# Kernel tuning notes

Measured on AMD Instinct MI355X. Metric: run time of the kernel, lower is better.

The kernel has to match this reference:

```python
import jax, jax.numpy as jnp
import numpy as np

N, F_IN, F_OUT = 8192, 512, 256


def setup_inputs() -> dict:
    key = jax.random.key(0)
    k1, k2, k3, k4 = jax.random.split(key, 4)
    x = jax.random.normal(k1, (N, F_IN), dtype=jnp.float32)
    adj = jax.random.randint(k2, (N, N), 0, 2, dtype=jnp.int32)
    # xavier_uniform with gain=1.414
    limW = 1.414 * np.sqrt(6.0 / (F_IN + F_OUT))
    W = jax.random.uniform(k3, (F_IN, F_OUT), dtype=jnp.float32, minval=-limW, maxval=limW)
    lima = 1.414 * np.sqrt(6.0 / (2 * F_OUT + 1))
    a = jax.random.uniform(k4, (2 * F_OUT, 1), dtype=jnp.float32, minval=-lima, maxval=lima)
    return {"x": x, "adj": adj, "W": W, "a": a}


def reference(x, adj, W, a):
    # h = x @ W : [N, F_out]
    h = x @ W
    f_out = h.shape[1]
    # additive score a^T [h_i ; h_j] is separable: (h @ a_l)_i + (h @ a_r)_j
    f_src = h @ a[:f_out, 0]   # [N]
    f_dst = h @ a[f_out:, 0]   # [N]
    e = jax.nn.leaky_relu(f_src[:, None] + f_dst[None, :], negative_slope=0.2)  # [N, N]
    e = jnp.where(adj > 0, e, jnp.float32(-9e15))
    attention = jax.nn.softmax(e, axis=1)  # row-wise over neighbors
    # dropout(p=0.6) is identity in eval mode
    h_prime = attention @ h  # [N, F_out]
    return h_prime
```

## Files before the change

kernel.cpp:

```cpp
#include <hip/hip_runtime.h>
#include <hip/hip_bf16.h>

#define NN 8192
#define FIN 512
#define FOUT 256

typedef __attribute__((ext_vector_type(8))) short short8;
typedef __attribute__((ext_vector_type(4))) short short4v;
typedef __attribute__((ext_vector_type(4))) float float4v;

__device__ __forceinline__ short f2bf(float f) {
    union { float f; unsigned u; } v; v.f = f;
    unsigned r = (v.u + 0x7FFFu + ((v.u >> 16) & 1u)) >> 16;
    return (short)r;
}
__device__ __forceinline__ float bf2f(short b) {
    union { unsigned u; float f; } v; v.u = ((unsigned)(unsigned short)b) << 16;
    return v.f;
}

__global__ __launch_bounds__(256) void wt_kernel(const float* __restrict__ W,
                                                 short* __restrict__ Wt) {
    int idx = blockIdx.x * 256 + threadIdx.x;
    int n = idx >> 9, k = idx & 511;
    Wt[idx] = f2bf(W[k * FOUT + n]);
}

__global__ __launch_bounds__(256) void h_kernel(const float* __restrict__ x,
                                                const short* __restrict__ Wt,
                                                short* __restrict__ h_t) {
    int wave = (blockIdx.x << 2) + (threadIdx.x >> 6);
    int lane = threadIdx.x & 63;
    int m0 = (wave & 511) << 4;
    int n0 = (wave >> 9) << 6;
    int lr = lane & 15, lq = lane >> 4;

    const float* xrow = x + (size_t)(m0 + lr) * FIN + lq * 8;
    const short* wbase = Wt + (size_t)(n0 + lr) * FIN + lq * 8;

    float4v acc[4] = {};
    for (int k0 = 0; k0 < FIN; k0 += 32) {
        float4v xa = *(const float4v*)(xrow + k0);
        float4v xb = *(const float4v*)(xrow + k0 + 4);
        short8 a;
        a[0] = f2bf(xa[0]); a[1] = f2bf(xa[1]); a[2] = f2bf(xa[2]); a[3] = f2bf(xa[3]);
        a[4] = f2bf(xb[0]); a[5] = f2bf(xb[1]); a[6] = f2bf(xb[2]); a[7] = f2bf(xb[3]);
#pragma unroll
        for (int ct = 0; ct < 4; ct++) {
            short8 b = *(const short8*)(wbase + (size_t)ct * 16 * FIN + k0);
            acc[ct] = __builtin_amdgcn_mfma_f32_16x16x32_bf16(a, b, acc[ct], 0, 0, 0);
        }
    }
#pragma unroll
    for (int ct = 0; ct < 4; ct++) {
#pragma unroll
        for (int reg = 0; reg < 4; reg++) {
            int m = m0 + lq * 4 + reg;
            int n = n0 + ct * 16 + lr;
            h_t[(size_t)n * NN + m] = f2bf(acc[ct][reg]);
        }
    }
}

__global__ __launch_bounds__(256) void f_kernel(const short* __restrict__ h_t,
                                                const float* __restrict__ a,
                                                float* __restrict__ f_src,
                                                float* __restrict__ f_dst) {
    int i = blockIdx.x * 256 + threadIdx.x;
    float s = 0.f, d = 0.f;
#pragma unroll 4
    for (int n = 0; n < FOUT; n++) {
        float hv = bf2f(h_t[(size_t)n * NN + i]);
        s = fmaf(hv, a[n], s);
        d = fmaf(hv, a[FOUT + n], d);
    }
    const float LOG2E = 1.4426950408889634f;
    f_src[i] = s * LOG2E;
    f_dst[i] = d * LOG2E;
}

__global__ __launch_bounds__(512) void gat_kernel(const int* __restrict__ adj,
                                                  const short* __restrict__ h_t,
                                                  const float* __restrict__ f_src,
                                                  const float* __restrict__ f_dst,
                                                  float* __restrict__ out) {
    __shared__ short Pt[32 * 72];
    __shared__ short Ht[256 * 72];
    __shared__ float l_sm[32];

    const int t = threadIdx.x;
    const int i0 = blockIdx.x * 32;
    const int r = t >> 4;
    const int c = t & 15;
    const int lane = t & 63;
    const int w = t >> 6;
    const int lr = lane & 15, lq = lane >> 4;
    const int n0 = w * 32;

    const float fs = f_src[i0 + r];
    const int* adjRow = adj + (size_t)(i0 + r) * NN + c * 4;

    float lpart = 0.f;
    float4v acc[2][2] = {};

    int4 av = *(const int4*)(adjRow);
    float4 fd = *(const float4*)(f_dst + c * 4);

    for (int j0 = 0; j0 < NN; j0 += 64) {
        float p[4];
        const float* fdp = (const float*)&fd;
        const int* avp = (const int*)&av;
#pragma unroll
        for (int q = 0; q < 4; q++) {
            float y = fs + fdp[q];
            y = fmaxf(y, 0.2f * y);
            float e = exp2f(y);
            p[q] = (avp[q] != 0) ? e : 0.f;
            lpart += p[q];
        }
        short4v pb;
        pb[0] = f2bf(p[0]); pb[1] = f2bf(p[1]); pb[2] = f2bf(p[2]); pb[3] = f2bf(p[3]);
        *(short4v*)&Pt[r * 72 + c * 4] = pb;

#pragma unroll
        for (int q = 0; q < 4; q++) {
            int c2 = t + q * 512;
            int n = c2 >> 3, ko = (c2 & 7) * 8;
            *(int4*)&Ht[n * 72 + ko] = *(const int4*)(h_t + (size_t)n * NN + j0 + ko);
        }

        if (j0 + 64 < NN) {
            av = *(const int4*)(adjRow + j0 + 64);
            fd = *(const float4*)(f_dst + j0 + 64 + c * 4);
        }
        __syncthreads();

#pragma unroll
        for (int kk = 0; kk < 2; kk++) {
            short8 a0 = *(const short8*)&Pt[lr * 72 + kk * 32 + lq * 8];
            short8 a1 = *(const short8*)&Pt[(16 + lr) * 72 + kk * 32 + lq * 8];
            short8 b0 = *(const short8*)&Ht[(n0 + lr) * 72 + kk * 32 + lq * 8];
            short8 b1 = *(const short8*)&Ht[(n0 + 16 + lr) * 72 + kk * 32 + lq * 8];
            acc[0][0] = __builtin_amdgcn_mfma_f32_16x16x32_bf16(a0, b0, acc[0][0], 0, 0, 0);
            acc[0][1] = __builtin_amdgcn_mfma_f32_16x16x32_bf16(a0, b1, acc[0][1], 0, 0, 0);
            acc[1][0] = __builtin_amdgcn_mfma_f32_16x16x32_bf16(a1, b0, acc[1][0], 0, 0, 0);
            acc[1][1] = __builtin_amdgcn_mfma_f32_16x16x32_bf16(a1, b1, acc[1][1], 0, 0, 0);
        }
        __syncthreads();
    }

#pragma unroll
    for (int off = 8; off >= 1; off >>= 1) lpart += __shfl_xor(lpart, off);
    if (c == 0) l_sm[r] = lpart;
    __syncthreads();

#pragma unroll
    for (int rt = 0; rt < 2; rt++) {
#pragma unroll
        for (int ct = 0; ct < 2; ct++) {
#pragma unroll
            for (int reg = 0; reg < 4; reg++) {
                int m = rt * 16 + lq * 4 + reg;
                int n = n0 + ct * 16 + lr;
                out[(size_t)(i0 + m) * FOUT + n] = acc[rt][ct][reg] / l_sm[m];
            }
        }
    }
}

extern "C" void kernel_launch(void* const* d_in, const int* in_sizes, int n_in,
                              void* d_out, int out_size, void* d_ws, size_t ws_size,
                              hipStream_t stream) {
    const float* x   = (const float*)d_in[0];
    const int*   adj = (const int*)d_in[1];
    const float* W   = (const float*)d_in[2];
    const float* a   = (const float*)d_in[3];
    float* out = (float*)d_out;

    char* ws = (char*)d_ws;
    short* h_t   = (short*)ws;
    short* Wt    = (short*)(ws + (4u << 20));
    float* f_src = (float*)(ws + (4u << 20) + (256u << 10));
    float* f_dst = (float*)(ws + (4u << 20) + (288u << 10));

    wt_kernel<<<512, 256, 0, stream>>>(W, Wt);
    h_kernel<<<512, 256, 0, stream>>>(x, Wt, h_t);
    f_kernel<<<NN / 256, 256, 0, stream>>>(h_t, a, f_src, f_dst);
    gat_kernel<<<NN / 32, 512, 0, stream>>>(adj, h_t, f_src, f_dst, out);
}
```

Measured before the change: 473.5 us.

## Split-K GAT aggregation with 64-row tiles, 32x32 MFMA, fused score projection

The main attention kernel now processes 64 query rows per block using 32x32x16 bf16 MFMAs. The neighbor dimension is split into up to four slices, with partial numerators and denominators written to workspace and summed by a new combine kernel. The f_src/f_dst projection is fused into the h GEMM epilogue using shuffles and atomics, removing a separate kernel. The W transpose now goes through shared memory so its accesses coalesce. The split adds partial-output traffic and an extra launch in exchange for more parallelism and higher reuse of h tiles across rows.

Measured after the change: 448.1 us. 1.06x faster.

```diff
diff --git a/kernel.cpp b/kernel.cpp
--- a/kernel.cpp
+++ b/kernel.cpp
@@ -4,31 +4,39 @@
 #define NN 8192
 #define FIN 512
 #define FOUT 256
+#define JTILE 64
 
 typedef __attribute__((ext_vector_type(8))) short short8;
 typedef __attribute__((ext_vector_type(4))) short short4v;
 typedef __attribute__((ext_vector_type(4))) float float4v;
+typedef __attribute__((ext_vector_type(16))) float float16v;
 
 __device__ __forceinline__ short f2bf(float f) {
     union { float f; unsigned u; } v; v.f = f;
     unsigned r = (v.u + 0x7FFFu + ((v.u >> 16) & 1u)) >> 16;
     return (short)r;
 }
-__device__ __forceinline__ float bf2f(short b) {
-    union { unsigned u; float f; } v; v.u = ((unsigned)(unsigned short)b) << 16;
-    return v.f;
-}
 
 __global__ __launch_bounds__(256) void wt_kernel(const float* __restrict__ W,
                                                  short* __restrict__ Wt) {
-    int idx = blockIdx.x * 256 + threadIdx.x;
-    int n = idx >> 9, k = idx & 511;
-    Wt[idx] = f2bf(W[k * FOUT + n]);
+    __shared__ short tile[32][33];
+    int tx = threadIdx.x & 31, ty = threadIdx.x >> 5;
+    int k0 = blockIdx.x * 32, n0 = blockIdx.y * 32;
+#pragma unroll
+    for (int r = 0; r < 32; r += 8)
+        tile[ty + r][tx] = f2bf(W[(size_t)(k0 + ty + r) * FOUT + n0 + tx]);
+    __syncthreads();
+#pragma unroll
+    for (int r = 0; r < 32; r += 8)
+        Wt[(size_t)(n0 + ty + r) * FIN + k0 + tx] = tile[tx][ty + r];
 }
 
 __global__ __launch_bounds__(256) void h_kernel(const float* __restrict__ x,
                                                 const short* __restrict__ Wt,
-                                                short* __restrict__ h_t) {
+                                                const float* __restrict__ a,
+                                                short* __restrict__ h_t,
+                                                float* __restrict__ f_src,
+                                                float* __restrict__ f_dst) {
     int wave = (blockIdx.x << 2) + (threadIdx.x >> 6);
     int lane = threadIdx.x & 63;
     int m0 = (wave & 511) << 4;
@@ -42,130 +50,164 @@
     for (int k0 = 0; k0 < FIN; k0 += 32) {
         float4v xa = *(const float4v*)(xrow + k0);
         float4v xb = *(const float4v*)(xrow + k0 + 4);
-        short8 a;
-        a[0] = f2bf(xa[0]); a[1] = f2bf(xa[1]); a[2] = f2bf(xa[2]); a[3] = f2bf(xa[3]);
-        a[4] = f2bf(xb[0]); a[5] = f2bf(xb[1]); a[6] = f2bf(xb[2]); a[7] = f2bf(xb[3]);
+        short8 av;
+        av[0] = f2bf(xa[0]); av[1] = f2bf(xa[1]); av[2] = f2bf(xa[2]); av[3] = f2bf(xa[3]);
+        av[4] = f2bf(xb[0]); av[5] = f2bf(xb[1]); av[6] = f2bf(xb[2]); av[7] = f2bf(xb[3]);
 #pragma unroll
         for (int ct = 0; ct < 4; ct++) {
-            short8 b = *(const short8*)(wbase + (size_t)ct * 16 * FIN + k0);
-            acc[ct] = __builtin_amdgcn_mfma_f32_16x16x32_bf16(a, b, acc[ct], 0, 0, 0);
-        }
-    }
+            short8 bv = *(const short8*)(wbase + (size_t)ct * 16 * FIN + k0);
+            acc[ct] = __builtin_amdgcn_mfma_f32_16x16x32_bf16(av, bv, acc[ct], 0, 0, 0);
+        }
+    }
+    float s_part[4] = {0.f, 0.f, 0.f, 0.f};
+    float d_part[4] = {0.f, 0.f, 0.f, 0.f};
 #pragma unroll
     for (int ct = 0; ct < 4; ct++) {
+        int n = n0 + ct * 16 + lr;
+        float al = a[n], ar = a[FOUT + n];
 #pragma unroll
         for (int reg = 0; reg < 4; reg++) {
-            int m = m0 + lq * 4 + reg;
-            int n = n0 + ct * 16 + lr;
-            h_t[(size_t)n * NN + m] = f2bf(acc[ct][reg]);
-        }
-    }
-}
-
-__global__ __launch_bounds__(256) void f_kernel(const short* __restrict__ h_t,
-                                                const float* __restrict__ a,
-                                                float* __restrict__ f_src,
-                                                float* __restrict__ f_dst) {
-    int i = blockIdx.x * 256 + threadIdx.x;
-    float s = 0.f, d = 0.f;
-#pragma unroll 4
-    for (int n = 0; n < FOUT; n++) {
-        float hv = bf2f(h_t[(size_t)n * NN + i]);
-        s = fmaf(hv, a[n], s);
-        d = fmaf(hv, a[FOUT + n], d);
+            float hv = acc[ct][reg];
+            s_part[reg] = fmaf(hv, al, s_part[reg]);
+            d_part[reg] = fmaf(hv, ar, d_part[reg]);
+            h_t[(size_t)n * NN + (m0 + lq * 4 + reg)] = f2bf(hv);
+        }
+    }
+#pragma unroll
+    for (int off = 1; off < 16; off <<= 1) {
+#pragma unroll
+        for (int reg = 0; reg < 4; reg++) {
+            s_part[reg] += __shfl_xor(s_part[reg], off);
+            d_part[reg] += __shfl_xor(d_part[reg], off);
+        }
     }
     const float LOG2E = 1.4426950408889634f;
-    f_src[i] = s * LOG2E;
-    f_dst[i] = d * LOG2E;
-}
-
-__global__ __launch_bounds__(512) void gat_kernel(const int* __restrict__ adj,
-                                                  const short* __restrict__ h_t,
-                                                  const float* __restrict__ f_src,
-                                                  const float* __restrict__ f_dst,
-                                                  float* __restrict__ out) {
-    __shared__ short Pt[32 * 72];
+    if (lr == 0) {
+#pragma unroll
+        for (int reg = 0; reg < 4; reg++) {
+            atomicAdd(&f_src[m0 + lq * 4 + reg], s_part[reg] * LOG2E);
+            atomicAdd(&f_dst[m0 + lq * 4 + reg], d_part[reg] * LOG2E);
+        }
+    }
+}
+
+__global__ __launch_bounds__(256, 2) void gat_kernel(const int* __restrict__ adj,
+                                                     const short* __restrict__ h_t,
+                                                     const float* __restrict__ f_src,
+                                                     const float* __restrict__ f_dst,
+                                                     float* __restrict__ Opart,
+                                                     float* __restrict__ lpart,
+                                                     int jlen) {
     __shared__ short Ht[256 * 72];
-    __shared__ float l_sm[32];
+    __shared__ short Pt[64 * 72];
+    __shared__ float Fd[2][64];
 
     const int t = threadIdx.x;
-    const int i0 = blockIdx.x * 32;
-    const int r = t >> 4;
-    const int c = t & 15;
-    const int lane = t & 63;
-    const int w = t >> 6;
-    const int lr = lane & 15, lq = lane >> 4;
-    const int n0 = w * 32;
-
-    const float fs = f_src[i0 + r];
-    const int* adjRow = adj + (size_t)(i0 + r) * NN + c * 4;
-
-    float lpart = 0.f;
-    float4v acc[2][2] = {};
-
-    int4 av = *(const int4*)(adjRow);
-    float4 fd = *(const float4*)(f_dst + c * 4);
-
-    for (int j0 = 0; j0 < NN; j0 += 64) {
-        float p[4];
-        const float* fdp = (const float*)&fd;
-        const int* avp = (const int*)&av;
-#pragma unroll
-        for (int q = 0; q < 4; q++) {
-            float y = fs + fdp[q];
-            y = fmaxf(y, 0.2f * y);
-            float e = exp2f(y);
-            p[q] = (avp[q] != 0) ? e : 0.f;
-            lpart += p[q];
-        }
-        short4v pb;
-        pb[0] = f2bf(p[0]); pb[1] = f2bf(p[1]); pb[2] = f2bf(p[2]); pb[3] = f2bf(p[3]);
-        *(short4v*)&Pt[r * 72 + c * 4] = pb;
-
-#pragma unroll
-        for (int q = 0; q < 4; q++) {
-            int c2 = t + q * 512;
-            int n = c2 >> 3, ko = (c2 & 7) * 8;
-            *(int4*)&Ht[n * 72 + ko] = *(const int4*)(h_t + (size_t)n * NN + j0 + ko);
-        }
-
-        if (j0 + 64 < NN) {
-            av = *(const int4*)(adjRow + j0 + 64);
-            fd = *(const float4*)(f_dst + j0 + 64 + c * 4);
+    const int i0 = blockIdx.x * 64;
+    const int slice = blockIdx.y;
+    const int jbase = slice * jlen;
+
+    const int prow = t >> 2, pjq = t & 3;
+    const int lane = t & 63, w = t >> 6;
+    const int l31 = lane & 31, lq = lane >> 5;
+    const int wn0 = w * 64;
+
+    const float fs = f_src[i0 + prow];
+    const int* adjRow = adj + (size_t)(i0 + prow) * NN;
+    const short* hrow = h_t + ((size_t)t << 13);
+
+    float16v acc00 = {}, acc01 = {}, acc10 = {}, acc11 = {};
+    float lp = 0.f;
+
+    if (t < 16) *(float4*)&Fd[0][t * 4] = *(const float4*)(f_dst + jbase + t * 4);
+    int4 av0 = *(const int4*)(adjRow + jbase + pjq * 16);
+    int4 av1 = *(const int4*)(adjRow + jbase + pjq * 16 + 4);
+    int4 av2 = *(const int4*)(adjRow + jbase + pjq * 16 + 8);
+    int4 av3 = *(const int4*)(adjRow + jbase + pjq * 16 + 12);
+    __syncthreads();
+
+    int buf = 0;
+    for (int jo = 0; jo < jlen; jo += JTILE) {
+        const int j0 = jbase + jo;
+        {
+            const float* fdc = &Fd[buf][pjq * 16];
+            short8 pbl, pbh;
+            int4 avs[4] = {av0, av1, av2, av3};
+#pragma unroll
+            for (int g = 0; g < 4; g++) {
+                const int* ai = (const int*)&avs[g];
+#pragma unroll
+                for (int q = 0; q < 4; q++) {
+                    float y = fs + fdc[g * 4 + q];
+                    y = fmaxf(y, 0.2f * y);
+                    float e = exp2f(y);
+                    float p = (ai[q] != 0) ? e : 0.f;
+                    lp += p;
+                    short pb = f2bf(p);
+                    if (g < 2) pbl[g * 4 + q] = pb; else pbh[(g - 2) * 4 + q] = pb;
+                }
+            }
+            *(short8*)&Pt[prow * 72 + pjq * 16] = pbl;
+            *(short8*)&Pt[prow * 72 + pjq * 16 + 8] = pbh;
+        }
+#pragma unroll
+        for (int q = 0; q < 8; q++)
+            *(short8*)&Ht[t * 72 + q * 8] = *(const short8*)(hrow + j0 + q * 8);
+
+        if (jo + JTILE < jlen) {
+            if (t < 16) *(float4*)&Fd[buf ^ 1][t * 4] = *(const float4*)(f_dst + j0 + JTILE + t * 4);
+            av0 = *(const int4*)(adjRow + j0 + JTILE + pjq * 16);
+            av1 = *(const int4*)(adjRow + j0 + JTILE + pjq * 16 + 4);
+            av2 = *(const int4*)(adjRow + j0 + JTILE + pjq * 16 + 8);
+            av3 = *(const int4*)(adjRow + j0 + JTILE + pjq * 16 + 12);
         }
         __syncthreads();
 
 #pragma unroll
-        for (int kk = 0; kk < 2; kk++) {
-            short8 a0 = *(const short8*)&Pt[lr * 72 + kk * 32 + lq * 8];
-            short8 a1 = *(const short8*)&Pt[(16 + lr) * 72 + kk * 32 + lq * 8];
-            short8 b0 = *(const short8*)&Ht[(n0 + lr) * 72 + kk * 32 + lq * 8];
-            short8 b1 = *(const short8*)&Ht[(n0 + 16 + lr) * 72 + kk * 32 + lq * 8];
-            acc[0][0] = __builtin_amdgcn_mfma_f32_16x16x32_bf16(a0, b0, acc[0][0], 0, 0, 0);
-            acc[0][1] = __builtin_amdgcn_mfma_f32_16x16x32_bf16(a0, b1, acc[0][1], 0, 0, 0);
-            acc[1][0] = __builtin_amdgcn_mfma_f32_16x16x32_bf16(a1, b0, acc[1][0], 0, 0, 0);
-            acc[1][1] = __builtin_amdgcn_mfma_f32_16x16x32_bf16(a1, b1, acc[1][1], 0, 0, 0);
-        }
+        for (int kk = 0; kk < 4; kk++) {
+            short8 a0 = *(const short8*)&Pt[l31 * 72 + kk * 16 + lq * 8];
+            short8 a1 = *(const short8*)&Pt[(32 + l31) * 72 + kk * 16 + lq * 8];
+            short8 b0 = *(const short8*)&Ht[(wn0 + l31) * 72 + kk * 16 + lq * 8];
+            short8 b1 = *(const short8*)&Ht[(wn0 + 32 + l31) * 72 + kk * 16 + lq * 8];
+            acc00 = __builtin_amdgcn_mfma_f32_32x32x16_bf16(a0, b0, acc00, 0, 0, 0);
+            acc01 = __builtin_amdgcn_mfma_f32_32x32x16_bf16(a0, b1, acc01, 0, 0, 0);
+            acc10 = __builtin_amdgcn_mfma_f32_32x32x16_bf16(a1, b0, acc10, 0, 0, 0);
+            acc11 = __builtin_amdgcn_mfma_f32_32x32x16_bf16(a1, b1, acc11, 0, 0, 0);
+        }
+        buf ^= 1;
         __syncthreads();
     }
 
-#pragma unroll
-    for (int off = 8; off >= 1; off >>= 1) lpart += __shfl_xor(lpart, off);
-    if (c == 0) l_sm[r] = lpart;
-    __syncthreads();
-
+    lp += __shfl_xor(lp, 1);
+    lp += __shfl_xor(lp, 2);
+    if (pjq == 0) lpart[slice * NN + i0 + prow] = lp;
+
+    float* obase = Opart + ((size_t)slice * NN + i0) * FOUT;
 #pragma unroll
     for (int rt = 0; rt < 2; rt++) {
 #pragma unroll
-        for (int ct = 0; ct < 2; ct++) {
-#pragma unroll
-            for (int reg = 0; reg < 4; reg++) {
-                int m = rt * 16 + lq * 4 + reg;
-                int n = n0 + ct * 16 + lr;
-                out[(size_t)(i0 + m) * FOUT + n] = acc[rt][ct][reg] / l_sm[m];
+        for (int nt = 0; nt < 2; nt++) {
+            const float16v& av = rt == 0 ? (nt == 0 ? acc00 : acc01) : (nt == 0 ? acc10 : acc11);
+#pragma unroll
+            for (int reg = 0; reg < 16; reg++) {
+                int row = rt * 32 + (reg & 3) + 8 * (reg >> 2) + 4 * lq;
+                int n = wn0 + nt * 32 + l31;
+                obase[(size_t)row * FOUT + n] = av[reg];
             }
         }
     }
+}
+
+__global__ __launch_bounds__(256) void combine_kernel(const float* __restrict__ Opart,
+                                                      const float* __restrict__ lpart,
+                                                      float* __restrict__ out, int slices) {
+    int i = blockIdx.x, n = threadIdx.x;
+    float o = 0.f, l = 0.f;
+    for (int s = 0; s < slices; s++) {
+        o += Opart[((size_t)s * NN + i) * FOUT + n];
+        l += lpart[s * NN + i];
+    }
+    out[(size_t)i * FOUT + n] = o / l;
 }
 
 extern "C" void kernel_launch(void* const* d_in, const int* in_sizes, int n_in,
@@ -182,9 +224,19 @@
     short* Wt    = (short*)(ws + (4u << 20));
     float* f_src = (float*)(ws + (4u << 20) + (256u << 10));
     float* f_dst = (float*)(ws + (4u << 20) + (288u << 10));
-
-    wt_kernel<<<512, 256, 0, stream>>>(W, Wt);
-    h_kernel<<<512, 256, 0, stream>>>(x, Wt, h_t);
-    f_kernel<<<NN / 256, 256, 0, stream>>>(h_t, a, f_src, f_dst);
-    gat_kernel<<<NN / 32, 512, 0, stream>>>(adj, h_t, f_src, f_dst, out);
-}
+    float* lpart = (float*)(ws + (4u << 20) + (320u << 10));
+    float* Opart = (float*)(ws + (5u << 20));
+
+    const size_t OSLICE = (size_t)NN * FOUT * 4;
+    int slices = 1;
+    if (ws_size >= (5u << 20) + 4 * OSLICE) slices = 4;
+    else if (ws_size >= (5u << 20) + 2 * OSLICE) slices = 2;
+    int jlen = NN / slices;
+
+    hipMemsetAsync(f_src, 0, 2 * NN * sizeof(float), stream);
+    wt_kernel<<<dim3(FIN / 32, FOUT / 32), 256, 0, stream>>>(W, Wt);
+    h_kernel<<<512, 256, 0, stream>>>(x, Wt, a, h_t, f_src, f_dst);
+    gat_kernel<<<dim3(NN / 64, slices), 256, 0, stream>>>(adj, h_t, f_src, f_dst,
+                                                          Opart, lpart, jlen);
+    combine_kernel<<<NN, 256, 0, stream>>>(Opart, lpart, out, slices);
+}
```
